# Performance work log

Hardware: AMD Instinct MI355X
Metric: run time of the kernel (lower is better)

## Reference

```python
import math
import jax, jax.numpy as jnp
import numpy as np

ORIG_FREQ = 16000
NEW_FREQ = 14400
LPF_WIDTH = 6


def _kaldi_weights(orig_freq, new_freq, lpf_width):
    """Kaldi LinearResample SetIndexesAndWeights (numpy, static)."""
    base = math.gcd(orig_freq, new_freq)
    output_samples = new_freq // base
    min_freq = min(orig_freq, new_freq)
    lowpass_cutoff = 0.99 * 0.5 * min_freq
    window_width = lpf_width / (2.0 * lowpass_cutoff)
    output_t = np.arange(output_samples, dtype=np.float64) / new_freq
    min_t = output_t - window_width
    max_t = output_t + window_width
    min_input_index = np.ceil(min_t * orig_freq)
    max_input_index = np.floor(max_t * orig_freq)
    num_indices = max_input_index - min_input_index + 1
    max_weight_width = int(num_indices.max())
    j = np.arange(max_weight_width, dtype=np.float64)
    input_index = min_input_index[:, None] + j[None, :]
    delta_t = input_index / orig_freq - output_t[:, None]
    weights = np.zeros_like(delta_t)
    inside = np.abs(delta_t) < window_width
    weights[inside] = 0.5 * (1 + np.cos(2 * math.pi * lowpass_cutoff / lpf_width * delta_t[inside]))
    t_zero = delta_t == 0.0
    t_nz = ~t_zero
    weights[t_nz] *= np.sin(2 * math.pi * lowpass_cutoff * delta_t[t_nz]) / (math.pi * delta_t[t_nz])
    weights[t_zero] *= 2 * lowpass_cutoff
    weights /= orig_freq
    return min_input_index.astype(np.int64), weights.astype(np.float32)


def _output_samples(input_num_samp, orig_freq, new_freq):
    tick_freq = abs(orig_freq * new_freq) // math.gcd(orig_freq, new_freq)
    ticks_per_input = tick_freq // orig_freq
    interval_length = input_num_samp * ticks_per_input
    if interval_length <= 0:
        return 0
    ticks_per_output = tick_freq // new_freq
    last = interval_length // ticks_per_output
    if last * ticks_per_output == interval_length:
        last -= 1
    return last + 1


def setup_inputs() -> dict:
    key = jax.random.key(0)
    waveforms = jax.random.normal(key, (64, 480000), dtype=jnp.float32)
    return {"waveforms": waveforms}


def reference(waveforms) -> jnp.ndarray:
    B, T = waveforms.shape
    base = math.gcd(ORIG_FREQ, NEW_FREQ)
    conv_stride = ORIG_FREQ // base          # input samples per unit (10)
    up = NEW_FREQ // base                    # output phases (9)
    first_indices, weights_np = _kaldi_weights(ORIG_FREQ, NEW_FREQ, LPF_WIDTH)
    window_size = weights_np.shape[1]
    tot_out = _output_samples(T, ORIG_FREQ, NEW_FREQ)
    max_index = (tot_out - 1) // up
    end_index = max_index * conv_stride + window_size

    x3 = waveforms[:, None, :]  # [B, 1, T]
    out = jnp.zeros((B, tot_out), dtype=waveforms.dtype)
    dn = jax.lax.conv_dimension_numbers((B, 1, T), (1, 1, window_size), ('NCH', 'OIH', 'NCH'))
    for i in range(up):
        fi = int(first_indices[i])
        start = max(0, fi)
        left_pad = max(0, -fi)
        cur_len = T - fi
        right_pad = max(0, end_index + 1 - cur_len)
        xw = jnp.pad(x3[..., start:], ((0, 0), (0, 0), (left_pad, right_pad)))
        ker = jnp.asarray(weights_np[i], dtype=waveforms.dtype)[None, None, :]
        cw = jax.lax.conv_general_dilated(xw, ker, (conv_stride,), 'VALID', dimension_numbers=dn)[:, 0, :]
        # place phase-i outputs at positions i, i+up, i+2*up, ... < tot_out
        count = (tot_out - i + up - 1) // up
        cw = cw[:, :count]
        if cw.shape[1] < count:
            cw = jnp.pad(cw, ((0, 0), (0, count - cw.shape[1])))
        out = out.at[:, i::up].add(cw)
    return out
```

## Files before the change

### kernel.cpp

```cpp
#include <hip/hip_runtime.h>
#include <math.h>

#define T_IN        480000
#define OUT_PER_ROW 432000
#define K_TOT       48000
#define PAIRS_PB    256
#define GROUPS_PB   (2 * PAIRS_PB)
#define OUT_LDS     (GROUPS_PB * 9)

struct ResampleW { float w[9][14]; };

__global__ __launch_bounds__(256)
void SpeedPerturb_resample_kernel(const float* __restrict__ in,
                                  float* __restrict__ out,
                                  ResampleW args)
{
    __shared__ float lout[OUT_LDS];
    const int row = blockIdx.y;
    const int k0  = blockIdx.x * GROUPS_PB;
    const int t   = threadIdx.x;
    const int kp  = (k0 >> 1) + t;
    const float* rin = in + (size_t)row * T_IN;

    const int al = 20 * kp - 8;
    float v[36];
    const bool interior = (blockIdx.x > 0) && (blockIdx.x < gridDim.x - 1);
    if (interior) {
        #pragma unroll
        for (int m = 0; m < 9; ++m) {
            float4 q = *reinterpret_cast<const float4*>(rin + al + 4 * m);
            v[4 * m + 0] = q.x; v[4 * m + 1] = q.y;
            v[4 * m + 2] = q.z; v[4 * m + 3] = q.w;
        }
    } else {
        #pragma unroll
        for (int m = 0; m < 36; ++m) {
            const int idx = al + m;
            v[m] = (idx >= 0 && idx < T_IN) ? rin[idx] : 0.f;
        }
    }

    constexpr int RB[9] = {0, 1, 2, 3, 4, 5, 6, 8, 9};

    #pragma unroll
    for (int g = 0; g < 2; ++g) {
        const int k = k0 + 2 * t + g;
        if (k < K_TOT) {
            #pragma unroll
            for (int i = 0; i < 9; ++i) {
                float s = 0.f;
                #pragma unroll
                for (int j = 0; j < 14; ++j)
                    s = fmaf(args.w[i][j], v[2 + 10 * g + RB[i] + j], s);
                lout[18 * t + 9 * g + i] = s;
            }
        }
    }
    __syncthreads();

    const int nout = min(OUT_LDS, (K_TOT - k0) * 9);
    float* obase = out + (size_t)row * OUT_PER_ROW + (size_t)k0 * 9;
    for (int q = t; q < (nout >> 2); q += 256) {
        *reinterpret_cast<float4*>(obase + 4 * q) =
            *reinterpret_cast<const float4*>(&lout[4 * q]);
    }
}

extern "C" void kernel_launch(void* const* d_in, const int* in_sizes, int n_in,
                              void* d_out, int out_size, void* d_ws, size_t ws_size,
                              hipStream_t stream) {
    const float* in  = (const float*)d_in[0];
    float*       out = (float*)d_out;
    const int B = out_size / OUT_PER_ROW;

    ResampleW args;
    const double orig = 16000.0;
    const double lowpass_cutoff = 0.99 * 0.5 * 14400.0;
    const double window_width = 6.0 / (2.0 * lowpass_cutoff);
    const double PI = 3.14159265358979323846;
    for (int i = 0; i < 9; ++i) {
        const double output_t = (double)i / 14400.0;
        const double min_input_index = ceil((output_t - window_width) * orig);
        for (int j = 0; j < 14; ++j) {
            const double delta_t = (min_input_index + j) / orig - output_t;
            double w = 0.0;
            if (fabs(delta_t) < window_width) {
                w = 0.5 * (1.0 + cos(2.0 * PI * lowpass_cutoff / 6.0 * delta_t));
                if (delta_t != 0.0)
                    w *= sin(2.0 * PI * lowpass_cutoff * delta_t) / (PI * delta_t);
                else
                    w *= 2.0 * lowpass_cutoff;
                w /= orig;
            }
            args.w[i][j] = (float)w;
        }
    }

    dim3 grid((K_TOT + GROUPS_PB - 1) / GROUPS_PB, B);
    SpeedPerturb_resample_kernel<<<grid, dim3(256), 0, stream>>>(in, out, args);
}
```

Measured before the change: 210.5 us.

## Use fixed persistent grid with software-pipelined loads and direct nontemporal stores

Switches from a 2D grid with one window per thread to a fixed 2048-block grid where each thread handles up to three flattened pairs, prefetching the next window's loads before computing the current one, with sched_barriers to keep that order. Output now goes straight to global memory as 8-byte nontemporal stores instead of being staged through LDS and written as coalesced float4s. The goal is to hide load latency and remove the LDS round-trip and __syncthreads. In exchange, register pressure rises from holding three 36-float windows, and each thread writes 72 contiguous bytes, so global writes are strided across lanes and less coalesced. It also hardcodes a batch of 64.

```diff
diff --git a/kernel.cpp b/kernel.cpp
--- a/kernel.cpp
+++ b/kernel.cpp
@@ -1,69 +1,97 @@
 #include <hip/hip_runtime.h>
 #include <math.h>
 
-#define T_IN        480000
-#define OUT_PER_ROW 432000
-#define K_TOT       48000
-#define PAIRS_PB    256
-#define GROUPS_PB   (2 * PAIRS_PB)
-#define OUT_LDS     (GROUPS_PB * 9)
+#define T_IN          480000
+#define OUT_PER_ROW   432000
+#define PAIRS_PER_ROW 24000
+#define TOT_PAIRS     (PAIRS_PER_ROW * 64)
+#define BLK           256
+#define NBLK          2048
+#define NTH           (BLK * NBLK)
+
+typedef float f32x4 __attribute__((ext_vector_type(4)));
+typedef float f32x2 __attribute__((ext_vector_type(2)));
 
 struct ResampleW { float w[9][14]; };
 
-__global__ __launch_bounds__(256)
+__device__ __forceinline__ void load_window(const float* __restrict__ in,
+                                            unsigned p, f32x4 r[9])
+{
+    const unsigned row = p / PAIRS_PER_ROW;
+    const int kp = (int)(p - row * PAIRS_PER_ROW);
+    const float* rin = in + (size_t)row * T_IN;
+    const int al = 20 * kp - 8;
+    if (kp >= 1 && kp <= PAIRS_PER_ROW - 2) {
+        #pragma unroll
+        for (int m = 0; m < 9; ++m)
+            r[m] = *reinterpret_cast<const f32x4*>(rin + al + 4 * m);
+    } else {
+        #pragma unroll
+        for (int m = 0; m < 9; ++m) {
+            #pragma unroll
+            for (int c = 0; c < 4; ++c) {
+                const int idx = al + 4 * m + c;
+                r[m][c] = (idx >= 0 && idx < T_IN) ? rin[idx] : 0.f;
+            }
+        }
+    }
+}
+
+__device__ __forceinline__ void compute_store(float* __restrict__ out,
+                                              unsigned p, const f32x4 r[9],
+                                              const ResampleW& args)
+{
+    const unsigned row = p / PAIRS_PER_ROW;
+    const int kp = (int)(p - row * PAIRS_PER_ROW);
+    float v[36];
+    #pragma unroll
+    for (int m = 0; m < 9; ++m) {
+        v[4*m+0] = r[m][0]; v[4*m+1] = r[m][1];
+        v[4*m+2] = r[m][2]; v[4*m+3] = r[m][3];
+    }
+    constexpr int RB[9] = {0, 1, 2, 3, 4, 5, 6, 8, 9};
+    float o[18];
+    #pragma unroll
+    for (int g = 0; g < 2; ++g) {
+        #pragma unroll
+        for (int i = 0; i < 9; ++i) {
+            float s = 0.f;
+            #pragma unroll
+            for (int j = 0; j < 14; ++j)
+                s = fmaf(args.w[i][j], v[2 + 10 * g + RB[i] + j], s);
+            o[9 * g + i] = s;
+        }
+    }
+    float* op = out + (size_t)row * OUT_PER_ROW + 18u * (size_t)kp;
+    #pragma unroll
+    for (int m = 0; m < 9; ++m) {
+        f32x2 t2; t2[0] = o[2*m]; t2[1] = o[2*m+1];
+        __builtin_nontemporal_store(t2, reinterpret_cast<f32x2*>(op + 2 * m));
+    }
+}
+
+__global__ __launch_bounds__(BLK)
 void SpeedPerturb_resample_kernel(const float* __restrict__ in,
                                   float* __restrict__ out,
                                   ResampleW args)
 {
-    __shared__ float lout[OUT_LDS];
-    const int row = blockIdx.y;
-    const int k0  = blockIdx.x * GROUPS_PB;
-    const int t   = threadIdx.x;
-    const int kp  = (k0 >> 1) + t;
-    const float* rin = in + (size_t)row * T_IN;
+    const unsigned tid = blockIdx.x * BLK + threadIdx.x;
+    const unsigned p0 = tid;
+    const unsigned p1 = tid + NTH;
+    const unsigned p2 = tid + 2u * NTH;
+    const bool has2 = p2 < TOT_PAIRS;
 
-    const int al = 20 * kp - 8;
-    float v[36];
-    const bool interior = (blockIdx.x > 0) && (blockIdx.x < gridDim.x - 1);
-    if (interior) {
-        #pragma unroll
-        for (int m = 0; m < 9; ++m) {
-            float4 q = *reinterpret_cast<const float4*>(rin + al + 4 * m);
-            v[4 * m + 0] = q.x; v[4 * m + 1] = q.y;
-            v[4 * m + 2] = q.z; v[4 * m + 3] = q.w;
-        }
-    } else {
-        #pragma unroll
-        for (int m = 0; m < 36; ++m) {
-            const int idx = al + m;
-            v[m] = (idx >= 0 && idx < T_IN) ? rin[idx] : 0.f;
-        }
-    }
+    f32x4 w0[9], w1[9], w2[9];
+    load_window(in, p0, w0);
+    load_window(in, p1, w1);
+    __builtin_amdgcn_sched_barrier(0);
 
-    constexpr int RB[9] = {0, 1, 2, 3, 4, 5, 6, 8, 9};
+    compute_store(out, p0, w0, args);
+    if (has2) load_window(in, p2, w2);
+    __builtin_amdgcn_sched_barrier(0);
 
-    #pragma unroll
-    for (int g = 0; g < 2; ++g) {
-        const int k = k0 + 2 * t + g;
-        if (k < K_TOT) {
-            #pragma unroll
-            for (int i = 0; i < 9; ++i) {
-                float s = 0.f;
-                #pragma unroll
-                for (int j = 0; j < 14; ++j)
-                    s = fmaf(args.w[i][j], v[2 + 10 * g + RB[i] + j], s);
-                lout[18 * t + 9 * g + i] = s;
-            }
-        }
-    }
-    __syncthreads();
-
-    const int nout = min(OUT_LDS, (K_TOT - k0) * 9);
-    float* obase = out + (size_t)row * OUT_PER_ROW + (size_t)k0 * 9;
-    for (int q = t; q < (nout >> 2); q += 256) {
-        *reinterpret_cast<float4*>(obase + 4 * q) =
-            *reinterpret_cast<const float4*>(&lout[4 * q]);
-    }
+    compute_store(out, p1, w1, args);
+    if (has2) compute_store(out, p2, w2, args);
 }
 
 extern "C" void kernel_launch(void* const* d_in, const int* in_sizes, int n_in,
@@ -71,7 +99,6 @@
                               hipStream_t stream) {
     const float* in  = (const float*)d_in[0];
     float*       out = (float*)d_out;
-    const int B = out_size / OUT_PER_ROW;
 
     ResampleW args;
     const double orig = 16000.0;
@@ -96,6 +123,5 @@
         }
     }
 
-    dim3 grid((K_TOT + GROUPS_PB - 1) / GROUPS_PB, B);
-    SpeedPerturb_resample_kernel<<<grid, dim3(256), 0, stream>>>(in, out, args);
+    SpeedPerturb_resample_kernel<<<dim3(NBLK), dim3(BLK), 0, stream>>>(in, out, args);
 }
```

Result: slower. 291.7 us (+38.6%).
